# Kernel tuning notes

Measured on AMD Instinct MI355X. Metric: run time of the kernel, lower is better.

Reference implementation:

```python
import jax, jax.numpy as jnp
import numpy as np

N_NODES = 50000
N_EDGES = 1600000
IN_FEATS = 256
ENC_H = 20
DEC_H = 64
BIAS = 0.0  # forward arg default
TEMPERATURE = 1.0


def setup_inputs() -> dict:
    key = jax.random.key(0)
    ks = jax.random.split(key, 8)
    x = jax.random.normal(ks[0], (N_NODES, IN_FEATS), dtype=jnp.float32)
    edge_index = jax.random.randint(ks[1], (2, N_EDGES), 0, N_NODES, dtype=jnp.int64)
    node_id = 42
    # GCNConv params (glorot-ish scale)
    W_gcn = jax.random.normal(ks[2], (IN_FEATS, ENC_H), dtype=jnp.float32) / np.sqrt(IN_FEATS)
    b_gcn = jnp.zeros((ENC_H,), dtype=jnp.float32)
    # decoder MLP params
    W1 = jax.random.normal(ks[3], (3 * ENC_H, DEC_H), dtype=jnp.float32) / np.sqrt(3 * ENC_H)
    b1 = jnp.zeros((DEC_H,), dtype=jnp.float32)
    W2 = jax.random.normal(ks[4], (DEC_H, 1), dtype=jnp.float32) / np.sqrt(DEC_H)
    b2 = jnp.zeros((1,), dtype=jnp.float32)
    return {"x": x, "edge_index": edge_index, "node_id": node_id,
            "W_gcn": W_gcn, "b_gcn": b_gcn, "W1": W1, "b1": b1, "W2": W2, "b2": b2}


def _gcn_conv(x, edge_index, W, b):
    """PyG GCNConv: add self loops, symmetric normalization, sum aggregation."""
    n = x.shape[0]
    xw = x @ W  # [N, ENC_H]
    loop = jnp.arange(n, dtype=edge_index.dtype)
    row = jnp.concatenate([edge_index[0], loop])  # source
    col = jnp.concatenate([edge_index[1], loop])  # target
    ones = jnp.ones(row.shape[0], dtype=x.dtype)
    deg = jax.ops.segment_sum(ones, col, num_segments=n)
    dinv = jnp.where(deg > 0, jax.lax.rsqrt(jnp.maximum(deg, 1e-12)), 0.0)
    norm = dinv[row] * dinv[col]  # [E+N]
    msgs = xw[row] * norm[:, None]
    out = jax.ops.segment_sum(msgs, col, num_segments=n)
    return out + b


def reference(x, edge_index, node_id, W_gcn, b_gcn, W1, b1, W2, b2):
    # encoder: GCN + ReLU
    enc = jax.nn.relu(_gcn_conv(x, edge_index, W_gcn, b_gcn))  # [N, ENC_H]
    # edge representation: [row_embed | col_embed | node_embed]
    rows, cols = edge_index[0], edge_index[1]
    node_embed = jnp.broadcast_to(enc[node_id], (rows.shape[0], enc.shape[1]))
    z = jnp.concatenate([enc[rows], enc[cols], node_embed], axis=1)  # [E, 3*ENC_H]
    # decoder MLP
    h = jax.nn.relu(z @ W1 + b1)
    out_dec = h @ W2 + b2  # [E, 1]
    # Gumbel-sigmoid sampling (training=True path)
    bias = BIAS + 0.0001
    u = jax.random.uniform(jax.random.key(123), out_dec.shape, dtype=out_dec.dtype)
    eps = (bias - (1.0 - bias)) * u + (1.0 - bias)  # in (bias, 1-bias)
    gate = jnp.log(eps) - jnp.log1p(-eps)
    return jax.nn.sigmoid((gate + out_dec) / TEMPERATURE)
```

## Files before the change

kernel.cpp:

```cpp
#include <hip/hip_runtime.h>
#include <hip/hip_bf16.h>

#define IN_FEATS 256
#define ENC_H    20
#define DEC_H    64
#define EPB      8192

__device__ __forceinline__ unsigned int rotl32(unsigned int x, int d) {
  return (x << d) | (x >> (32 - d));
}

__device__ __forceinline__ void threefry2x32(unsigned int k0, unsigned int k1,
                                             unsigned int x0, unsigned int x1,
                                             unsigned int& o0, unsigned int& o1) {
  unsigned int ks0 = k0, ks1 = k1, ks2 = k0 ^ k1 ^ 0x1BD11BDAu;
  x0 += ks0; x1 += ks1;
  x0 += x1; x1 = rotl32(x1, 13); x1 ^= x0;
  x0 += x1; x1 = rotl32(x1, 15); x1 ^= x0;
  x0 += x1; x1 = rotl32(x1, 26); x1 ^= x0;
  x0 += x1; x1 = rotl32(x1,  6); x1 ^= x0;
  x0 += ks1; x1 += ks2 + 1u;
  x0 += x1; x1 = rotl32(x1, 17); x1 ^= x0;
  x0 += x1; x1 = rotl32(x1, 29); x1 ^= x0;
  x0 += x1; x1 = rotl32(x1, 16); x1 ^= x0;
  x0 += x1; x1 = rotl32(x1, 24); x1 ^= x0;
  x0 += ks2; x1 += ks0 + 2u;
  x0 += x1; x1 = rotl32(x1, 13); x1 ^= x0;
  x0 += x1; x1 = rotl32(x1, 15); x1 ^= x0;
  x0 += x1; x1 = rotl32(x1, 26); x1 ^= x0;
  x0 += x1; x1 = rotl32(x1,  6); x1 ^= x0;
  x0 += ks0; x1 += ks1 + 3u;
  x0 += x1; x1 = rotl32(x1, 17); x1 ^= x0;
  x0 += x1; x1 = rotl32(x1, 29); x1 ^= x0;
  x0 += x1; x1 = rotl32(x1, 16); x1 ^= x0;
  x0 += x1; x1 = rotl32(x1, 24); x1 ^= x0;
  x0 += ks1; x1 += ks2 + 4u;
  x0 += x1; x1 = rotl32(x1, 13); x1 ^= x0;
  x0 += x1; x1 = rotl32(x1, 15); x1 ^= x0;
  x0 += x1; x1 = rotl32(x1, 26); x1 ^= x0;
  x0 += x1; x1 = rotl32(x1,  6); x1 ^= x0;
  x0 += ks2; x1 += ks0 + 5u;
  o0 = x0; o1 = x1;
}

__device__ __forceinline__ float2 bf2_unpack(unsigned int u) {
  float2 f;
  f.x = __uint_as_float(u << 16);
  f.y = __uint_as_float(u & 0xffff0000u);
  return f;
}


__global__ __launch_bounds__(1024) void k_binhist(const int* __restrict__ col,
                                                  int* __restrict__ bbc, int E, int nbins) {
  __shared__ int h[256];
  int t = threadIdx.x;
  if (t < 256) h[t] = 0;
  __syncthreads();
  int lo = blockIdx.x * EPB;
  int hi = min(lo + EPB, E);
  for (int e = lo + t; e < hi; e += 1024) atomicAdd(&h[col[e] >> 8], 1);
  __syncthreads();
  if (t < nbins) bbc[blockIdx.x * nbins + t] = h[t];
}

__global__ void k_colA(const int* __restrict__ bbc, int* __restrict__ base,
                       int* __restrict__ binTot, int nblk, int nbins) {
  __shared__ int sd[256];
  int t = threadIdx.x;
  int bin = blockIdx.x;
  int v = (t < nblk) ? bbc[(size_t)t * nbins + bin] : 0;
  sd[t] = v;
  __syncthreads();
#pragma unroll
  for (int off = 1; off < 256; off <<= 1) {
    int tmp = (t >= off) ? sd[t - off] : 0;
    __syncthreads();
    sd[t] += tmp;
    __syncthreads();
  }
  if (t < nblk) base[(size_t)t * nbins + bin] = sd[t] - v;
  if (t == 255) binTot[bin] = sd[255];
}

__global__ void k_colB(const int* __restrict__ binTot, int* __restrict__ binStart, int nbins) {
  __shared__ int sd[256];
  int t = threadIdx.x;
  int v = (t < nbins) ? binTot[t] : 0;
  sd[t] = v;
  __syncthreads();
#pragma unroll
  for (int off = 1; off < 256; off <<= 1) {
    int tmp = (t >= off) ? sd[t - off] : 0;
    __syncthreads();
    sd[t] += tmp;
    __syncthreads();
  }
  if (t < nbins) {
    binStart[t] = sd[t] - v;
    if (t == nbins - 1) binStart[nbins] = sd[t];
  }
}

__global__ __launch_bounds__(1024) void k_binscatter(const int* __restrict__ row,
                                                     const int* __restrict__ col,
                                                     const int* __restrict__ base,
                                                     const int* __restrict__ binStart,
                                                     unsigned int* __restrict__ binned,
                                                     int* __restrict__ einv,
                                                     int E, int nbins) {
  __shared__ int cur[256];
  int t = threadIdx.x;
  if (t < nbins) cur[t] = binStart[t] + base[(size_t)blockIdx.x * nbins + t];
  __syncthreads();
  int lo = blockIdx.x * EPB;
  int hi = min(lo + EPB, E);
  for (int e = lo + t; e < hi; e += 1024) {
    int c = col[e];
    int slot = atomicAdd(&cur[c >> 8], 1);
    binned[slot] = (unsigned int)row[e] | ((unsigned int)c << 16);
    einv[e] = slot;
  }
}

__global__ __launch_bounds__(1024) void k_binsort(const unsigned int* __restrict__ binned,
                                                  const int* __restrict__ binStart,
                                                  unsigned short* __restrict__ sorted_r,
                                                  int* __restrict__ nstart,
                                                  float* __restrict__ dinv,
                                                  int N, int E) {
  __shared__ int cnt[256];
  __shared__ int ls[256];
  __shared__ int cur[256];
  int t = threadIdx.x;
  int bin = blockIdx.x;
  if (t < 256) cnt[t] = 0;
  __syncthreads();
  int s = binStart[bin], epos = binStart[bin + 1];
  for (int i = s + t; i < epos; i += 1024)
    atomicAdd(&cnt[(binned[i] >> 16) & 0xFFu], 1);
  __syncthreads();
  int v = (t < 256) ? cnt[t] : 0;
  if (t < 256) ls[t] = v;
  __syncthreads();
#pragma unroll
  for (int off = 1; off < 256; off <<= 1) {
    int tmp = 0;
    if (t < 256 && t >= off) tmp = ls[t - off];
    __syncthreads();
    if (t < 256 && t >= off) ls[t] += tmp;
    __syncthreads();
  }
  if (t < 256) {
    int ex = ls[t] - v;
    cur[t] = s + ex;
    int n = (bin << 8) + t;
    if (n < N) {
      nstart[n] = s + ex;
      dinv[n] = rsqrtf((float)(v + 1));
    }
  }
  if (bin == 0 && t == 0) nstart[N] = E;
  __syncthreads();
  for (int i = s + t; i < epos; i += 1024) {
    unsigned int e32 = binned[i];
    int cl = (int)((e32 >> 16) & 0xFFu);
    int slot = atomicAdd(&cur[cl], 1);
    sorted_r[slot] = (unsigned short)(e32 & 0xFFFFu);
  }
}


__global__ void k_xw(const float* __restrict__ x, const float* __restrict__ W,
                     const float* __restrict__ dinv, __hip_bfloat16* __restrict__ xwd, int N) {
  __shared__ float Wl[IN_FEATS * ENC_H];
  for (int i = threadIdx.x; i < IN_FEATS * ENC_H; i += blockDim.x) Wl[i] = W[i];
  __syncthreads();
  int g = blockIdx.x * blockDim.x + threadIdx.x;
  int n = g >> 2, part = g & 3;
  if (n >= N) return;
  float acc[ENC_H];
#pragma unroll
  for (int j = 0; j < ENC_H; j++) acc[j] = 0.0f;
  const float4* x4 = reinterpret_cast<const float4*>(x + (size_t)n * IN_FEATS);
#pragma unroll 4
  for (int k4 = 0; k4 < 16; k4++) {
    float4 v = x4[k4 * 4 + part];
    int kbase = k4 * 16 + part * 4;
    const float* w0 = &Wl[(kbase + 0) * ENC_H];
    const float* w1 = &Wl[(kbase + 1) * ENC_H];
    const float* w2 = &Wl[(kbase + 2) * ENC_H];
    const float* w3 = &Wl[(kbase + 3) * ENC_H];
#pragma unroll
    for (int j = 0; j < ENC_H; j++) {
      acc[j] = fmaf(v.x, w0[j], acc[j]);
      acc[j] = fmaf(v.y, w1[j], acc[j]);
      acc[j] = fmaf(v.z, w2[j], acc[j]);
      acc[j] = fmaf(v.w, w3[j], acc[j]);
    }
  }
#pragma unroll
  for (int j = 0; j < ENC_H; j++) acc[j] += __shfl_xor(acc[j], 1);
#pragma unroll
  for (int j = 0; j < ENC_H; j++) acc[j] += __shfl_xor(acc[j], 2);
  float d = dinv[n];
  __hip_bfloat16* o = xwd + (size_t)n * ENC_H;
  int jb = part * 5;
#pragma unroll
  for (int jj = 0; jj < 5; jj++) o[jb + jj] = __float2bfloat16(acc[jb + jj] * d);
}

__global__ void k_gather(const int* __restrict__ nstart,
                         const unsigned short* __restrict__ sorted_r,
                         const __hip_bfloat16* __restrict__ xwd, const float* __restrict__ dinv,
                         const float* __restrict__ bg, float* __restrict__ enc, int N) {
  int t = blockIdx.x * blockDim.x + threadIdx.x;
  int n = t / ENC_H;
  int j = t % ENC_H;
  if (n >= N) return;
  int s = nstart[n], epos = nstart[n + 1];
  float acc = __bfloat162float(xwd[(size_t)n * ENC_H + j]);
  for (int k = s; k < epos; k++) {
    int r = (int)sorted_r[k];
    acc += __bfloat162float(xwd[(size_t)r * ENC_H + j]);
  }
  float v = acc * dinv[n] + bg[j];
  enc[(size_t)n * ENC_H + j] = fmaxf(v, 0.0f);
}

__global__ void k_pq(const float* __restrict__ enc, const float* __restrict__ W1,
                     __hip_bfloat16* __restrict__ P1, __hip_bfloat16* __restrict__ P2,
                     __hip_bfloat16* __restrict__ Q1, __hip_bfloat16* __restrict__ Q2, int N) {
  __shared__ float Wl[2 * ENC_H * DEC_H];
  for (int i = threadIdx.x; i < 2 * ENC_H * DEC_H; i += blockDim.x) Wl[i] = W1[i];
  __syncthreads();
  int t = blockIdx.x * blockDim.x + threadIdx.x;
  int n = t / DEC_H, j = t % DEC_H;
  if (n >= N) return;
  const float* en = enc + (size_t)n * ENC_H;
  float p = 0.0f, q = 0.0f;
#pragma unroll
  for (int k = 0; k < ENC_H; k++) {
    float ev = en[k];
    p = fmaf(ev, Wl[k * DEC_H + j], p);
    q = fmaf(ev, Wl[(k + ENC_H) * DEC_H + j], q);
  }
  size_t idx = (size_t)n * 32 + (j & 31);
  if (j < 32) { P1[idx] = __float2bfloat16(p); Q1[idx] = __float2bfloat16(q); }
  else        { P2[idx] = __float2bfloat16(p); Q2[idx] = __float2bfloat16(q); }
}

__global__ void k_t3(const float* __restrict__ enc, const float* __restrict__ W1,
                     const float* __restrict__ b1, const int* __restrict__ node_id,
                     float* __restrict__ t3) {
  int j = threadIdx.x;
  int nid = node_id[0];
  const float* en = enc + (size_t)nid * ENC_H;
  float a = b1[j];
#pragma unroll
  for (int k = 0; k < ENC_H; k++) a = fmaf(en[k], W1[(2 * ENC_H + k) * DEC_H + j], a);
  t3[j] = a;
}

template <int HALF>
__global__ void k_dec_half(const unsigned int* __restrict__ binned,
                           const __hip_bfloat16* __restrict__ Ph,
                           const __hip_bfloat16* __restrict__ Qh,
                           const float* __restrict__ t3, const float* __restrict__ W2,
                           const float* __restrict__ b2,
                           float* __restrict__ partial, int E) {
  __shared__ float t3l[32], w2l[32];
  if (threadIdx.x < 32) {
    t3l[threadIdx.x] = t3[HALF * 32 + threadIdx.x];
    w2l[threadIdx.x] = W2[HALF * 32 + threadIdx.x];
  }
  __syncthreads();
  int pos = blockIdx.x * blockDim.x + threadIdx.x;
  if (pos >= E) return;
  unsigned int v = binned[pos];
  int r = (int)(v & 0xFFFFu);
  int c = (int)(v >> 16);
  const uint4* pr = reinterpret_cast<const uint4*>(Ph + (size_t)r * 32);
  const uint4* qc = reinterpret_cast<const uint4*>(Qh + (size_t)c * 32);
  float acc = 0.0f;
#pragma unroll
  for (int b = 0; b < 4; b++) {
    uint4 pu = pr[b];
    uint4 qu = qc[b];
    int j0 = b * 8;
    float2 p0 = bf2_unpack(pu.x), q0 = bf2_unpack(qu.x);
    float2 p1 = bf2_unpack(pu.y), q1 = bf2_unpack(qu.y);
    float2 p2 = bf2_unpack(pu.z), q2 = bf2_unpack(qu.z);
    float2 p3 = bf2_unpack(pu.w), q3 = bf2_unpack(qu.w);
    float h;
    h = fmaxf(p0.x + q0.x + t3l[j0 + 0], 0.0f); acc = fmaf(h, w2l[j0 + 0], acc);
    h = fmaxf(p0.y + q0.y + t3l[j0 + 1], 0.0f); acc = fmaf(h, w2l[j0 + 1], acc);
    h = fmaxf(p1.x + q1.x + t3l[j0 + 2], 0.0f); acc = fmaf(h, w2l[j0 + 2], acc);
    h = fmaxf(p1.y + q1.y + t3l[j0 + 3], 0.0f); acc = fmaf(h, w2l[j0 + 3], acc);
    h = fmaxf(p2.x + q2.x + t3l[j0 + 4], 0.0f); acc = fmaf(h, w2l[j0 + 4], acc);
    h = fmaxf(p2.y + q2.y + t3l[j0 + 5], 0.0f); acc = fmaf(h, w2l[j0 + 5], acc);
    h = fmaxf(p3.x + q3.x + t3l[j0 + 6], 0.0f); acc = fmaf(h, w2l[j0 + 6], acc);
    h = fmaxf(p3.y + q3.y + t3l[j0 + 7], 0.0f); acc = fmaf(h, w2l[j0 + 7], acc);
  }
  if (HALF == 0) {
    partial[pos] = acc;
  } else {
    partial[pos] += acc + b2[0];
  }
}

__global__ void k_final(const int* __restrict__ einv, const float* __restrict__ partial,
                        float* __restrict__ out, int E) {
  int e = blockIdx.x * blockDim.x + threadIdx.x;
  if (e >= E) return;
  float od = partial[einv[e]];
  unsigned int o0, o1;
  threefry2x32(0u, 123u, 0u, (unsigned int)e, o0, o1);
  unsigned int bits = o0 ^ o1;
  float u = __uint_as_float((bits >> 9) | 0x3f800000u) - 1.0f;
  float eps = (-0.9998f) * u + 0.9999f;
  float gate = logf(eps) - log1pf(-eps);
  float s = 1.0f / (1.0f + expf(-(gate + od)));
  out[e] = s;
}

extern "C" void kernel_launch(void* const* d_in, const int* in_sizes, int n_in,
                              void* d_out, int out_size, void* d_ws, size_t ws_size,
                              hipStream_t stream) {
  const float* x       = (const float*)d_in[0];
  const int*   edge    = (const int*)d_in[1];
  const int*   node_id = (const int*)d_in[2];
  const float* W_gcn   = (const float*)d_in[3];
  const float* b_gcn   = (const float*)d_in[4];
  const float* W1      = (const float*)d_in[5];
  const float* b1      = (const float*)d_in[6];
  const float* W2      = (const float*)d_in[7];
  const float* b2      = (const float*)d_in[8];
  float* out = (float*)d_out;

  int N = in_sizes[0] / IN_FEATS;
  int E = in_sizes[1] / 2;
  const int* erow = edge;
  const int* ecol = edge + E;
  int nbins = (N + 255) >> 8;
  int NB = (E + EPB - 1) / EPB;

  char* ws = (char*)d_ws;
  size_t off = 0;
  auto alloc = [&](size_t bytes) {
    char* p = ws + off;
    off = (off + bytes + 255) & ~(size_t)255;
    return p;
  };
  __hip_bfloat16* xwd = (__hip_bfloat16*)alloc((size_t)N * ENC_H * sizeof(__hip_bfloat16));
  float* enc  = (float*)alloc((size_t)N * ENC_H * sizeof(float));
  float* dinv = (float*)alloc((size_t)N * sizeof(float));
  int*  nstart = (int*)alloc((size_t)(N + 1) * sizeof(int));
  unsigned int*   binned   = (unsigned int*)alloc((size_t)E * sizeof(unsigned int));
  int*            einv     = (int*)alloc((size_t)E * sizeof(int));
  unsigned short* sorted_r = (unsigned short*)alloc((size_t)E * sizeof(unsigned short));
  int* bbc      = (int*)alloc((size_t)NB * nbins * sizeof(int));
  int* base     = (int*)alloc((size_t)NB * nbins * sizeof(int));
  int* binTot   = (int*)alloc((size_t)nbins * sizeof(int));
  int* binStart = (int*)alloc((size_t)(nbins + 1) * sizeof(int));
  __hip_bfloat16* P1 = (__hip_bfloat16*)alloc((size_t)N * 32 * sizeof(__hip_bfloat16));
  __hip_bfloat16* P2 = (__hip_bfloat16*)alloc((size_t)N * 32 * sizeof(__hip_bfloat16));
  __hip_bfloat16* Q1 = (__hip_bfloat16*)alloc((size_t)N * 32 * sizeof(__hip_bfloat16));
  __hip_bfloat16* Q2 = (__hip_bfloat16*)alloc((size_t)N * 32 * sizeof(__hip_bfloat16));
  float* partial = (float*)alloc((size_t)E * sizeof(float));
  float* t3   = (float*)alloc((size_t)DEC_H * sizeof(float));
  (void)ws_size; (void)n_in; (void)out_size;

  const int B = 256;
  int ge  = (E + B - 1) / B;
  int gxw = (N * 4 + B - 1) / B;
  int gg  = (N * ENC_H + B - 1) / B;
  int gpq = (N * DEC_H + B - 1) / B;

  k_binhist   <<<NB, 1024, 0, stream>>>(ecol, bbc, E, nbins);
  k_colA      <<<nbins, 256, 0, stream>>>(bbc, base, binTot, NB, nbins);
  k_colB      <<<1, 256, 0, stream>>>(binTot, binStart, nbins);
  k_binscatter<<<NB, 1024, 0, stream>>>(erow, ecol, base, binStart, binned, einv, E, nbins);
  k_binsort   <<<nbins, 1024, 0, stream>>>(binned, binStart, sorted_r, nstart, dinv, N, E);
  k_xw        <<<gxw, B, 0, stream>>>(x, W_gcn, dinv, xwd, N);
  k_gather    <<<gg, B, 0, stream>>>(nstart, sorted_r, xwd, dinv, b_gcn, enc, N);
  k_pq        <<<gpq, B, 0, stream>>>(enc, W1, P1, P2, Q1, Q2, N);
  k_t3        <<<1, DEC_H, 0, stream>>>(enc, W1, b1, node_id, t3);
  k_dec_half<0><<<ge, B, 0, stream>>>(binned, P1, Q1, t3, W2, b2, partial, E);
  k_dec_half<1><<<ge, B, 0, stream>>>(binned, P2, Q2, t3, W2, b2, partial, E);
  k_final     <<<ge, B, 0, stream>>>(einv, partial, out, E);
}
```

Measured before the change: 187.5 us.

## Use nontemporal loads/stores, vectorize gather, and store decoder partials as bf16

Adds nontemporal load/store hints to streaming edge arrays across the sort, decoder, and final kernels so they bypass cache retention. The gather kernel now has each thread accumulate 4 features via 8-byte vector loads, using 5 threads per node instead of 20. The decoder partial sum buffer is cut from fp32 to bf16, halving its traffic at the cost of extra rounding of the logit before the sigmoid. The bf16 rounding of intermediate logits adds precision risk to the output.

```diff
diff --git a/kernel.cpp b/kernel.cpp
--- a/kernel.cpp
+++ b/kernel.cpp
@@ -5,6 +5,9 @@
 #define ENC_H    20
 #define DEC_H    64
 #define EPB      8192
+
+#define NT_LOAD(x)     __builtin_nontemporal_load(&(x))
+#define NT_STORE(x, v) __builtin_nontemporal_store((v), &(x))
 
 __device__ __forceinline__ unsigned int rotl32(unsigned int x, int d) {
   return (x << d) | (x >> (32 - d));
@@ -50,6 +53,11 @@
   return f;
 }
 
+__device__ __forceinline__ unsigned short bf16_bits(float f) {
+  __hip_bfloat16 h = __float2bfloat16(f);
+  return *reinterpret_cast<unsigned short*>(&h);
+}
+
 
 __global__ __launch_bounds__(1024) void k_binhist(const int* __restrict__ col,
                                                   int* __restrict__ bbc, int E, int nbins) {
@@ -59,7 +67,7 @@
   __syncthreads();
   int lo = blockIdx.x * EPB;
   int hi = min(lo + EPB, E);
-  for (int e = lo + t; e < hi; e += 1024) atomicAdd(&h[col[e] >> 8], 1);
+  for (int e = lo + t; e < hi; e += 1024) atomicAdd(&h[NT_LOAD(col[e]) >> 8], 1);
   __syncthreads();
   if (t < nbins) bbc[blockIdx.x * nbins + t] = h[t];
 }
@@ -116,10 +124,11 @@
   int lo = blockIdx.x * EPB;
   int hi = min(lo + EPB, E);
   for (int e = lo + t; e < hi; e += 1024) {
-    int c = col[e];
+    int c = NT_LOAD(col[e]);
+    int r = NT_LOAD(row[e]);
     int slot = atomicAdd(&cur[c >> 8], 1);
-    binned[slot] = (unsigned int)row[e] | ((unsigned int)c << 16);
-    einv[e] = slot;
+    NT_STORE(binned[slot], (unsigned int)r | ((unsigned int)c << 16));
+    NT_STORE(einv[e], slot);
   }
 }
 
@@ -138,7 +147,7 @@
   __syncthreads();
   int s = binStart[bin], epos = binStart[bin + 1];
   for (int i = s + t; i < epos; i += 1024)
-    atomicAdd(&cnt[(binned[i] >> 16) & 0xFFu], 1);
+    atomicAdd(&cnt[(NT_LOAD(binned[i]) >> 16) & 0xFFu], 1);
   __syncthreads();
   int v = (t < 256) ? cnt[t] : 0;
   if (t < 256) ls[t] = v;
@@ -163,10 +172,10 @@
   if (bin == 0 && t == 0) nstart[N] = E;
   __syncthreads();
   for (int i = s + t; i < epos; i += 1024) {
-    unsigned int e32 = binned[i];
+    unsigned int e32 = NT_LOAD(binned[i]);
     int cl = (int)((e32 >> 16) & 0xFFu);
     int slot = atomicAdd(&cur[cl], 1);
-    sorted_r[slot] = (unsigned short)(e32 & 0xFFFFu);
+    NT_STORE(sorted_r[slot], (unsigned short)(e32 & 0xFFFFu));
   }
 }
 
@@ -215,17 +224,28 @@
                          const __hip_bfloat16* __restrict__ xwd, const float* __restrict__ dinv,
                          const float* __restrict__ bg, float* __restrict__ enc, int N) {
   int t = blockIdx.x * blockDim.x + threadIdx.x;
-  int n = t / ENC_H;
-  int j = t % ENC_H;
+  int n = t / 5;
+  int lane5 = t - n * 5;
   if (n >= N) return;
+  int jb = lane5 * 4;
+  const char* xwb = (const char*)xwd;
+  uint2 sv = *reinterpret_cast<const uint2*>(xwb + (size_t)n * 40 + lane5 * 8);
+  float2 a01 = bf2_unpack(sv.x), a23 = bf2_unpack(sv.y);
+  float f0 = a01.x, f1 = a01.y, f2 = a23.x, f3 = a23.y;
   int s = nstart[n], epos = nstart[n + 1];
-  float acc = __bfloat162float(xwd[(size_t)n * ENC_H + j]);
   for (int k = s; k < epos; k++) {
-    int r = (int)sorted_r[k];
-    acc += __bfloat162float(xwd[(size_t)r * ENC_H + j]);
-  }
-  float v = acc * dinv[n] + bg[j];
-  enc[(size_t)n * ENC_H + j] = fmaxf(v, 0.0f);
+    int r = (int)NT_LOAD(sorted_r[k]);
+    uint2 v = *reinterpret_cast<const uint2*>(xwb + (size_t)r * 40 + lane5 * 8);
+    float2 b01 = bf2_unpack(v.x), b23 = bf2_unpack(v.y);
+    f0 += b01.x; f1 += b01.y; f2 += b23.x; f3 += b23.y;
+  }
+  float d = dinv[n];
+  float4 o;
+  o.x = fmaxf(f0 * d + bg[jb + 0], 0.0f);
+  o.y = fmaxf(f1 * d + bg[jb + 1], 0.0f);
+  o.z = fmaxf(f2 * d + bg[jb + 2], 0.0f);
+  o.w = fmaxf(f3 * d + bg[jb + 3], 0.0f);
+  *reinterpret_cast<float4*>(enc + (size_t)n * ENC_H + jb) = o;
 }
 
 __global__ void k_pq(const float* __restrict__ enc, const float* __restrict__ W1,
@@ -268,7 +288,7 @@
                            const __hip_bfloat16* __restrict__ Qh,
                            const float* __restrict__ t3, const float* __restrict__ W2,
                            const float* __restrict__ b2,
-                           float* __restrict__ partial, int E) {
+                           unsigned short* __restrict__ partial, int E) {
   __shared__ float t3l[32], w2l[32];
   if (threadIdx.x < 32) {
     t3l[threadIdx.x] = t3[HALF * 32 + threadIdx.x];
@@ -277,7 +297,7 @@
   __syncthreads();
   int pos = blockIdx.x * blockDim.x + threadIdx.x;
   if (pos >= E) return;
-  unsigned int v = binned[pos];
+  unsigned int v = NT_LOAD(binned[pos]);
   int r = (int)(v & 0xFFFFu);
   int c = (int)(v >> 16);
   const uint4* pr = reinterpret_cast<const uint4*>(Ph + (size_t)r * 32);
@@ -303,17 +323,19 @@
     h = fmaxf(p3.y + q3.y + t3l[j0 + 7], 0.0f); acc = fmaf(h, w2l[j0 + 7], acc);
   }
   if (HALF == 0) {
-    partial[pos] = acc;
+    NT_STORE(partial[pos], bf16_bits(acc));
   } else {
-    partial[pos] += acc + b2[0];
-  }
-}
-
-__global__ void k_final(const int* __restrict__ einv, const float* __restrict__ partial,
+    float prev = __uint_as_float((unsigned int)NT_LOAD(partial[pos]) << 16);
+    float od = acc + prev + b2[0];
+    NT_STORE(partial[pos], bf16_bits(od));
+  }
+}
+
+__global__ void k_final(const int* __restrict__ einv, const unsigned short* __restrict__ partial,
                         float* __restrict__ out, int E) {
   int e = blockIdx.x * blockDim.x + threadIdx.x;
   if (e >= E) return;
-  float od = partial[einv[e]];
+  float od = __uint_as_float((unsigned int)partial[NT_LOAD(einv[e])] << 16);
   unsigned int o0, o1;
   threefry2x32(0u, 123u, 0u, (unsigned int)e, o0, o1);
   unsigned int bits = o0 ^ o1;
@@ -321,7 +343,7 @@
   float eps = (-0.9998f) * u + 0.9999f;
   float gate = logf(eps) - log1pf(-eps);
   float s = 1.0f / (1.0f + expf(-(gate + od)));
-  out[e] = s;
+  NT_STORE(out[e], s);
 }
 
 extern "C" void kernel_launch(void* const* d_in, const int* in_sizes, int n_in,
@@ -367,14 +389,14 @@
   __hip_bfloat16* P2 = (__hip_bfloat16*)alloc((size_t)N * 32 * sizeof(__hip_bfloat16));
   __hip_bfloat16* Q1 = (__hip_bfloat16*)alloc((size_t)N * 32 * sizeof(__hip_bfloat16));
   __hip_bfloat16* Q2 = (__hip_bfloat16*)alloc((size_t)N * 32 * sizeof(__hip_bfloat16));
-  float* partial = (float*)alloc((size_t)E * sizeof(float));
+  unsigned short* partial = (unsigned short*)alloc((size_t)E * sizeof(unsigned short));
   float* t3   = (float*)alloc((size_t)DEC_H * sizeof(float));
   (void)ws_size; (void)n_in; (void)out_size;
 
   const int B = 256;
   int ge  = (E + B - 1) / B;
   int gxw = (N * 4 + B - 1) / B;
-  int gg  = (N * ENC_H + B - 1) / B;
+  int gg  = (N * 5 + B - 1) / B;
   int gpq = (N * DEC_H + B - 1) / B;
 
   k_binhist   <<<NB, 1024, 0, stream>>>(ecol, bbc, E, nbins);
```

Measured after the change: 259.8 us. 1.39x slower.
